# Performance work log

Hardware: AMD Instinct MI355X
Metric: run time of the kernel (lower is better)

The kernel has to match this reference:

```python
import jax, jax.numpy as jnp
import numpy as np

T, B, DIM = 64, 16, 512
H, Dh, ETA = 8, 64, 4
FD = ETA * Dh  # feature_dim = 256
EPS = 1e-6


def setup_inputs() -> dict:
    key = jax.random.key(0)
    ks = jax.random.split(key, 12)

    def w(k, o, i):
        return jax.random.normal(k, (o, i), jnp.float32) * (1.0 / np.sqrt(i).astype(np.float32))

    return {
        "inputs": jax.random.normal(ks[0], (T, B, DIM), jnp.float32),
        "terminations": jax.random.randint(ks[1], (T, B), 0, 2).astype(jnp.int32),
        "kv_state_prev": jnp.zeros((B, H, FD, Dh), jnp.float32),
        "norm_state_prev": jnp.zeros((B, H, FD), jnp.float32),
        "Wq": w(ks[2], H * Dh, DIM),
        "Wk": w(ks[3], H * Dh, DIM),
        "Wv": w(ks[4], H * Dh, DIM),
        "Wb": w(ks[5], H * Dh, DIM),
        "Wg": w(ks[6], H * Dh, DIM),
        "Wp1": w(ks[7], H * ETA, DIM),
        "Wp2": w(ks[8], H * ETA, DIM),
        "Wp3": w(ks[9], H * ETA, DIM),
        "Wo": w(ks[10], DIM, H * Dh),
        "bo": jnp.zeros((DIM,), jnp.float32),
    }


def reference(inputs, terminations, kv_state_prev, norm_state_prev,
              Wq, Wk, Wv, Wb, Wg, Wp1, Wp2, Wp3, Wo, bo):
    def proj(W, e):
        return (inputs @ W.T).reshape(T, B, H, e)

    q = proj(Wq, Dh)
    k = proj(Wk, Dh)
    v = proj(Wv, Dh)
    beta = jax.nn.sigmoid(proj(Wb, Dh))
    gamma = jax.nn.sigmoid(proj(Wg, Dh))
    p1 = proj(Wp1, ETA)
    p2 = proj(Wp2, ETA)
    p3 = proj(Wp3, ETA)

    # feature map: outer product of relu(p) [eta] and x [head_dim] -> [eta*head_dim]
    def fmap(x, p):
        return jnp.einsum('tbhe,tbhd->tbhed', jax.nn.relu(p), x).reshape(T, B, H, FD)

    phi_q = fmap(q, p2)
    psi_k = fmap(k, p1)
    # gamma map: outer product of sigmoid(p3) and sigmoid-gated gamma, values in (0,1)
    gamma_feat = jnp.einsum('tbhe,tbhd->tbhed', jax.nn.sigmoid(p3), gamma).reshape(T, B, H, FD)

    gated_v = v * beta                       # [T,B,H,Dh]
    gated_k = psi_k * gamma_feat             # [T,B,H,FD]

    term_mask = (1.0 - terminations.astype(jnp.float32))[:, :, None, None]  # [T,B,1,1]
    discount = (1.0 - gamma_feat) * term_mask  # [T,B,H,FD]

    kv_upd = jnp.einsum('tbhd,tbhD->tbhDd', gated_v, gated_k)  # [T,B,H,FD,Dh]

    def step(carry, x):
        kv, nm = carry
        d, u_kv, u_nm = x
        kv = d[..., None] * kv + u_kv
        nm = d * nm + u_nm
        return (kv, nm), (kv, nm)

    _, (kv_all, nm_all) = jax.lax.scan(step, (kv_state_prev, norm_state_prev),
                                       (discount, kv_upd, gated_k))

    attn_num = jnp.einsum('tbhDd,tbhD->tbhd', kv_all, phi_q)
    attn_den = jnp.einsum('tbhD,tbhD->tbh', phi_q, nm_all)
    attn_out = (attn_num / (attn_den[..., None] + EPS)).reshape(T, B, H * Dh)
    output = attn_out @ Wo.T + bo
    return (output, kv_all[-1], nm_all[-1])
```

## Files before the change

kernel.cpp:

```cpp
#include <hip/hip_runtime.h>


#define T_N   64
#define B_N   16
#define DIM_N 512
#define H_N   8
#define DH_N  64

#define OUT_ELEMS   524288
#define KV_ELEMS    2097152
#define PROJ_ELEMS  2719744

typedef _Float16 f16;
typedef f16   f16x8 __attribute__((ext_vector_type(8)));
typedef float f32x4 __attribute__((ext_vector_type(4)));

__device__ __forceinline__ float sigmoidf_(float x) {
    return 1.0f / (1.0f + __expf(-x));
}

template <int CTRL, int RM>
__device__ __forceinline__ float dpp_add_(float x) {
    int mv = __builtin_amdgcn_update_dpp(__float_as_int(x), __float_as_int(x),
                                         CTRL, RM, 0xF, false);
    return x + __int_as_float(mv);
}
__device__ __forceinline__ float half_reduce_dpp(float x) {
    x = dpp_add_<0xB1, 0xF>(x);
    x = dpp_add_<0x4E, 0xF>(x);
    x = dpp_add_<0x141, 0xF>(x);
    x = dpp_add_<0x140, 0xF>(x);
    x = dpp_add_<0x142, 0xA>(x);
    return x;
}

__device__ __forceinline__ void gemm64_core(const float* __restrict__ A,
                                            const float* __restrict__ W,
                                            const float* __restrict__ bias,
                                            float* __restrict__ C, int N,
                                            int mb, int nb, int kBase, int kLen) {
    const int nbase = nb * 64;
    if (nbase >= N) return;

    __shared__ float As[2][16][68];
    __shared__ float Bs[2][16][68];

    const int tid = threadIdx.x;
    const int mbase = mb * 64;
    const int tx = tid & 15;
    const int ty = tid >> 4;
    const int sr = tid >> 2;
    const int sk = (tid & 3) << 2;
    const bool wok = (nbase + sr) < N;

    const float* Ap = A + (size_t)(mbase + sr) * 512 + kBase + sk;
    const float* Wp = W + (size_t)(nbase + sr) * 512 + kBase + sk;

    float4 av = *(const float4*)Ap;
    float4 wv = wok ? *(const float4*)Wp : make_float4(0.f, 0.f, 0.f, 0.f);
    As[0][sk + 0][sr] = av.x; As[0][sk + 1][sr] = av.y;
    As[0][sk + 2][sr] = av.z; As[0][sk + 3][sr] = av.w;
    Bs[0][sk + 0][sr] = wv.x; Bs[0][sk + 1][sr] = wv.y;
    Bs[0][sk + 2][sr] = wv.z; Bs[0][sk + 3][sr] = wv.w;

    float acc[4][4];
    #pragma unroll
    for (int i = 0; i < 4; ++i)
        #pragma unroll
        for (int j = 0; j < 4; ++j) acc[i][j] = 0.f;

    for (int k0 = 0; k0 < kLen; k0 += 16) {
        const int buf = (k0 >> 4) & 1;
        __syncthreads();
        const bool more = (k0 + 16) < kLen;
        if (more) {
            av = *(const float4*)(Ap + k0 + 16);
            wv = wok ? *(const float4*)(Wp + k0 + 16) : make_float4(0.f, 0.f, 0.f, 0.f);
        }
        #pragma unroll
        for (int k = 0; k < 16; ++k) {
            float4 a  = *(const float4*)&As[buf][k][ty << 2];
            float4 bq = *(const float4*)&Bs[buf][k][tx << 2];
            float ar[4] = {a.x, a.y, a.z, a.w};
            float br[4] = {bq.x, bq.y, bq.z, bq.w};
            #pragma unroll
            for (int i = 0; i < 4; ++i)
                #pragma unroll
                for (int j = 0; j < 4; ++j)
                    acc[i][j] = fmaf(ar[i], br[j], acc[i][j]);
        }
        if (more) {
            const int nbuf = buf ^ 1;
            As[nbuf][sk + 0][sr] = av.x; As[nbuf][sk + 1][sr] = av.y;
            As[nbuf][sk + 2][sr] = av.z; As[nbuf][sk + 3][sr] = av.w;
            Bs[nbuf][sk + 0][sr] = wv.x; Bs[nbuf][sk + 1][sr] = wv.y;
            Bs[nbuf][sk + 2][sr] = wv.z; Bs[nbuf][sk + 3][sr] = wv.w;
        }
    }

    #pragma unroll
    for (int i = 0; i < 4; ++i) {
        const int m = mbase + (ty << 2) + i;
        #pragma unroll
        for (int j = 0; j < 4; ++j) {
            const int n = nbase + (tx << 2) + j;
            if (n < N) {
                float v = acc[i][j];
                if (bias) v += bias[n];
                C[(size_t)m * N + n] = v;
            }
        }
    }
}

struct ProjW {
    const float* W[8];
    float*       D[8];
};

__device__ __forceinline__ void cvt_split_store(f16* __restrict__ dh,
                                                f16* __restrict__ dl,
                                                float4 v0, float4 v1) {
    float x[8] = {v0.x, v0.y, v0.z, v0.w, v1.x, v1.y, v1.z, v1.w};
    f16x8 h, lo;
    #pragma unroll
    for (int e = 0; e < 8; ++e) {
        f16 hh = (f16)x[e];
        h[e]  = hh;
        lo[e] = (f16)(x[e] - (float)hh);
    }
    *(f16x8*)dh = h;
    *(f16x8*)dl = lo;
}

__global__ __launch_bounds__(256) void proj_mfma_kernel(const float* __restrict__ X,
                                                        ProjW a) {
    const int id = blockIdx.x;
    const int z = id & 7;
    const int rem = id >> 3;
    const int mb = rem & 15;
    const int nb = rem >> 4;
    const int N = (z < 5) ? 512 : 32;
    const int nbase = nb * 64;
    if (nbase >= N) return;

    const float* __restrict__ W = a.W[z];
    float* __restrict__ C = a.D[z];
    const int mbase = mb * 64;

    __shared__ f16 AsH[2][64][40];
    __shared__ f16 AsL[2][64][40];
    __shared__ f16 BsH[2][64][40];
    __shared__ f16 BsL[2][64][40];

    const int tid = threadIdx.x;
    const int sr = tid >> 2;
    const int kq = (tid & 3) << 3;
    const bool wok = (nbase + sr) < N;
    const float* Ap = X + (size_t)(mbase + sr) * 512 + kq;
    const float* Wp = W + (size_t)(nbase + sr) * 512 + kq;

    const int l  = tid & 63;
    const int w  = tid >> 6;
    const int wr = (w >> 1) << 5;
    const int wc = (w & 1) << 5;
    const int lr = l & 15;
    const int lk = (l >> 4) << 3;

    f32x4 acc[2][2] = {};

    float4 xa0 = *(const float4*)(Ap);
    float4 xa1 = *(const float4*)(Ap + 4);
    float4 wb0 = wok ? *(const float4*)(Wp)     : make_float4(0.f, 0.f, 0.f, 0.f);
    float4 wb1 = wok ? *(const float4*)(Wp + 4) : make_float4(0.f, 0.f, 0.f, 0.f);
    cvt_split_store(&AsH[0][sr][kq], &AsL[0][sr][kq], xa0, xa1);
    cvt_split_store(&BsH[0][sr][kq], &BsL[0][sr][kq], wb0, wb1);

    for (int k0 = 0; k0 < 512; k0 += 32) {
        const int buf = (k0 >> 5) & 1;
        __syncthreads();
        const bool more = (k0 + 32) < 512;
        if (more) {
            xa0 = *(const float4*)(Ap + k0 + 32);
            xa1 = *(const float4*)(Ap + k0 + 36);
            wb0 = wok ? *(const float4*)(Wp + k0 + 32) : make_float4(0.f, 0.f, 0.f, 0.f);
            wb1 = wok ? *(const float4*)(Wp + k0 + 36) : make_float4(0.f, 0.f, 0.f, 0.f);
        }

        f16x8 aH[2], aL[2], bH[2], bL[2];
        #pragma unroll
        for (int i = 0; i < 2; ++i) {
            const int row = wr + i * 16 + lr;
            aH[i] = *(const f16x8*)&AsH[buf][row][lk];
            aL[i] = *(const f16x8*)&AsL[buf][row][lk];
        }
        #pragma unroll
        for (int j = 0; j < 2; ++j) {
            const int col = wc + j * 16 + lr;
            bH[j] = *(const f16x8*)&BsH[buf][col][lk];
            bL[j] = *(const f16x8*)&BsL[buf][col][lk];
        }

        #pragma unroll
        for (int i = 0; i < 2; ++i)
            #pragma unroll
            for (int j = 0; j < 2; ++j) {
                acc[i][j] = __builtin_amdgcn_mfma_f32_16x16x32_f16(aH[i], bH[j], acc[i][j], 0, 0, 0);
                acc[i][j] = __builtin_amdgcn_mfma_f32_16x16x32_f16(aH[i], bL[j], acc[i][j], 0, 0, 0);
                acc[i][j] = __builtin_amdgcn_mfma_f32_16x16x32_f16(aL[i], bH[j], acc[i][j], 0, 0, 0);
            }

        if (more) {
            const int nbuf = buf ^ 1;
            cvt_split_store(&AsH[nbuf][sr][kq], &AsL[nbuf][sr][kq], xa0, xa1);
            cvt_split_store(&BsH[nbuf][sr][kq], &BsL[nbuf][sr][kq], wb0, wb1);
        }
    }

    #pragma unroll
    for (int j = 0; j < 2; ++j) {
        const int n = nbase + wc + j * 16 + lr;
        if (n < N) {
            #pragma unroll
            for (int i = 0; i < 2; ++i) {
                #pragma unroll
                for (int q = 0; q < 4; ++q) {
                    const int m = mbase + wr + i * 16 + ((l >> 4) << 2) + q;
                    C[(size_t)m * N + n] = acc[i][j][q];
                }
            }
        }
    }
}

__global__ __launch_bounds__(256) void out_gemm_kernel(const float* __restrict__ A,
                                                       const float* __restrict__ W,
                                                       const float* __restrict__ bias,
                                                       float* __restrict__ C) {
    gemm64_core(A, W, bias, C, 512, blockIdx.x, blockIdx.y, 0, 512);
}

struct OutP { float* P[4]; };
__global__ __launch_bounds__(256) void out_partial_kernel(const float* __restrict__ A,
                                                          const float* __restrict__ W,
                                                          OutP p) {
    const int id = blockIdx.x;
    const int m = id & 15;
    const int n = (id >> 4) & 7;
    const int kq = id >> 7;
    gemm64_core(A, W, nullptr, p.P[kq], 512, m, n, kq * 128, 128);
}

__global__ __launch_bounds__(256) void out_reduce_kernel(
    const float* __restrict__ p0, const float* __restrict__ p1,
    const float* __restrict__ p2, const float* __restrict__ p3,
    const float* __restrict__ bias, float* __restrict__ out) {
    const int i = blockIdx.x * 256 + threadIdx.x;
    float4 a = ((const float4*)p0)[i];
    float4 b = ((const float4*)p1)[i];
    float4 c = ((const float4*)p2)[i];
    float4 d = ((const float4*)p3)[i];
    float4 bv = ((const float4*)bias)[i & 127];
    float4 r;
    r.x = a.x + b.x + c.x + d.x + bv.x;
    r.y = a.y + b.y + c.y + d.y + bv.y;
    r.z = a.z + b.z + c.z + d.z + bv.z;
    r.w = a.w + b.w + c.w + d.w + bv.w;
    ((float4*)out)[i] = r;
}

__global__ __launch_bounds__(256) void gate_kernel(
    const float* __restrict__ qb,  const float* __restrict__ kb,
    const float* __restrict__ vb,  const float* __restrict__ bb,
    const float* __restrict__ gb,  const float* __restrict__ p1b,
    const float* __restrict__ p2b, const float* __restrict__ p3b,
    const int* __restrict__ term,
    float* __restrict__ disc_g, float* __restrict__ gk_g,
    float* __restrict__ phiq_g, float* __restrict__ gv_g) {
    const int h = blockIdx.x;
    const int row = blockIdx.y;
    const int D = threadIdx.x;
    const int e = D >> 6, di = D & 63;
    const size_t base = (size_t)row * 512 + h * 64;
    const size_t pb = (size_t)row * 32 + h * 4;

    float q = qb[base + di], k = kb[base + di], g = gb[base + di];
    float p1 = p1b[pb + e], p2 = p2b[pb + e], p3 = p3b[pb + e];
    float mask = 1.0f - (float)term[row];
    float gf = sigmoidf_(p3) * sigmoidf_(g);

    const size_t o = ((size_t)row * 8 + h) * 256 + D;
    disc_g[o] = (1.0f - gf) * mask;
    gk_g[o]   = fmaxf(p1, 0.f) * k * gf;
    phiq_g[o] = fmaxf(p2, 0.f) * q;
    if (D < 64)
        gv_g[((size_t)row * 8 + h) * 64 + D] = vb[base + D] * sigmoidf_(bb[base + D]);
}

__global__ __launch_bounds__(256) void scan8_kernel(
    const float* __restrict__ disc_g, const float* __restrict__ gk_g,
    const float* __restrict__ phiq_g, const float* __restrict__ gv_g,
    float* __restrict__ vb ,
    const float* __restrict__ kv0, const float* __restrict__ nm0,
    float* __restrict__ dout) {
    const int blk = blockIdx.x;
    const int bh = blk & 127;
    const int s  = blk >> 7;
    const int b  = bh >> 3;
    const int h  = bh & 7;
    const int tid = threadIdx.x;
    const int w = tid >> 6;
    const int l = tid & 63;
    const int half = l >> 5;
    const int li = l & 31;
    const int d0 = s * 16 + w * 4 + half * 2;
    const int D0 = li << 3;

    float kv[8][2];
    float nm[8];
    {
        const float* kp = kv0 + ((size_t)bh * 256 + D0) * 64 + d0;
        #pragma unroll
        for (int j = 0; j < 8; ++j) {
            float2 r = *(const float2*)(kp + (size_t)j * 64);
            kv[j][0] = r.x; kv[j][1] = r.y;
        }
        float4 na  = *(const float4*)(nm0 + (size_t)bh * 256 + D0);
        float4 nb_ = *(const float4*)(nm0 + (size_t)bh * 256 + D0 + 4);
        nm[0] = na.x; nm[1] = na.y; nm[2] = na.z; nm[3] = na.w;
        nm[4] = nb_.x; nm[5] = nb_.y; nm[6] = nb_.z; nm[7] = nb_.w;
    }

    float4 cd0, cd1, cg0, cg1, cp0, cp1; float2 cgv;
    {
        const size_t go = ((size_t)b * 8 + h) * 256 + D0;
        cd0 = *(const float4*)(disc_g + go);  cd1 = *(const float4*)(disc_g + go + 4);
        cg0 = *(const float4*)(gk_g + go);    cg1 = *(const float4*)(gk_g + go + 4);
        cp0 = *(const float4*)(phiq_g + go);  cp1 = *(const float4*)(phiq_g + go + 4);
        cgv = *(const float2*)(gv_g + ((size_t)b * 8 + h) * 64 + d0);
    }

    for (int t = 0; t < T_N; ++t) {
        const int row = t * B_N + b;
        const size_t base = (size_t)row * 512 + h * 64;

        float4 nd0 = {}, nd1 = {}, ng0 = {}, ng1 = {}, np0 = {}, np1 = {};
        float2 ngv = {};
        if (t + 1 < T_N) {
            const size_t go2 = ((size_t)(row + B_N) * 8 + h) * 256 + D0;
            nd0 = *(const float4*)(disc_g + go2); nd1 = *(const float4*)(disc_g + go2 + 4);
            ng0 = *(const float4*)(gk_g + go2);   ng1 = *(const float4*)(gk_g + go2 + 4);
            np0 = *(const float4*)(phiq_g + go2); np1 = *(const float4*)(phiq_g + go2 + 4);
            ngv = *(const float2*)(gv_g + ((size_t)(row + B_N) * 8 + h) * 64 + d0);
        }

        const float dj[8]  = {cd0.x, cd0.y, cd0.z, cd0.w, cd1.x, cd1.y, cd1.z, cd1.w};
        const float gkj[8] = {cg0.x, cg0.y, cg0.z, cg0.w, cg1.x, cg1.y, cg1.z, cg1.w};
        const float phj[8] = {cp0.x, cp0.y, cp0.z, cp0.w, cp1.x, cp1.y, cp1.z, cp1.w};

        float den = 0.f, n0 = 0.f, n1 = 0.f;
        #pragma unroll
        for (int j = 0; j < 8; ++j) {
            nm[j] = dj[j] * nm[j] + gkj[j];
            den = fmaf(phj[j], nm[j], den);
            kv[j][0] = dj[j] * kv[j][0] + gkj[j] * cgv.x; n0 = fmaf(phj[j], kv[j][0], n0);
            kv[j][1] = dj[j] * kv[j][1] + gkj[j] * cgv.y; n1 = fmaf(phj[j], kv[j][1], n1);
        }

        n0  = half_reduce_dpp(n0);
        n1  = half_reduce_dpp(n1);
        den = half_reduce_dpp(den);

        if (li == 16) {
            vb[base + d0]     = n0 / (den + 1e-6f);
            vb[base + d0 + 1] = n1 / (den + 1e-6f);
        }

        cd0 = nd0; cd1 = nd1; cg0 = ng0; cg1 = ng1; cp0 = np0; cp1 = np1; cgv = ngv;
    }

    {
        float* kp = dout + OUT_ELEMS + ((size_t)bh * 256 + D0) * 64 + d0;
        #pragma unroll
        for (int j = 0; j < 8; ++j)
            *(float2*)(kp + (size_t)j * 64) = make_float2(kv[j][0], kv[j][1]);
        if (s == 0 && w == 0 && half == 0) {
            float* np = dout + OUT_ELEMS + KV_ELEMS + (size_t)bh * 256 + D0;
            *(float4*)np       = make_float4(nm[0], nm[1], nm[2], nm[3]);
            *(float4*)(np + 4) = make_float4(nm[4], nm[5], nm[6], nm[7]);
        }
    }
}

extern "C" void kernel_launch(void* const* d_in, const int* in_sizes, int n_in,
                              void* d_out, int out_size, void* d_ws, size_t ws_size,
                              hipStream_t stream) {
    (void)in_sizes; (void)n_in; (void)out_size;

    const float* X    = (const float*)d_in[0];
    const int*   term = (const int*)  d_in[1];
    const float* kv0  = (const float*)d_in[2];
    const float* nm0  = (const float*)d_in[3];
    const float* Wo   = (const float*)d_in[12];
    const float* bo   = (const float*)d_in[13];

    float* out = (float*)d_out;

    float* qb  = (float*)d_ws;
    float* kb  = qb  + 524288;
    float* vb  = kb  + 524288;
    float* bb  = vb  + 524288;
    float* gb  = bb  + 524288;
    float* p1b = gb  + 524288;
    float* p2b = p1b + 32768;
    float* p3b = p2b + 32768;
    float* disc_g = p3b + 32768;
    float* gk_g   = disc_g + 2097152;
    float* phiq_g = gk_g   + 2097152;
    float* gv_g   = phiq_g + 2097152;
    const size_t need_bytes = (size_t)(PROJ_ELEMS + 6815744) * 4;
    const bool big = ws_size >= need_bytes;

    ProjW pa;
    pa.W[0] = (const float*)d_in[4];  pa.W[1] = (const float*)d_in[5];
    pa.W[2] = (const float*)d_in[6];  pa.W[3] = (const float*)d_in[7];
    pa.W[4] = (const float*)d_in[8];  pa.W[5] = (const float*)d_in[9];
    pa.W[6] = (const float*)d_in[10]; pa.W[7] = (const float*)d_in[11];
    pa.D[0] = qb;  pa.D[1] = kb;  pa.D[2] = vb;  pa.D[3] = bb;
    pa.D[4] = gb;  pa.D[5] = p1b; pa.D[6] = p2b; pa.D[7] = p3b;
    proj_mfma_kernel<<<1024, 256, 0, stream>>>(X, pa);

    gate_kernel<<<dim3(8, 1024), 256, 0, stream>>>(qb, kb, vb, bb, gb,
                                                   p1b, p2b, p3b, term,
                                                   disc_g, gk_g, phiq_g, gv_g);
    scan8_kernel<<<512, 256, 0, stream>>>(disc_g, gk_g, phiq_g, gv_g,
                                          vb, kv0, nm0, out);
    if (big) {
        OutP op; op.P[0] = qb; op.P[1] = kb; op.P[2] = bb; op.P[3] = gb;
        out_partial_kernel<<<512, 256, 0, stream>>>(vb, Wo, op);
        out_reduce_kernel<<<512, 256, 0, stream>>>(qb, kb, bb, gb, bo, out);
    } else {
        out_gemm_kernel<<<dim3(16, 8), 256, 0, stream>>>(vb, Wo, bo, out);
    }
}
```

Baseline: 175.8 us.

## Fuse gate computation into scan kernel via double-buffered shared memory

```diff
diff --git a/kernel.cpp b/kernel.cpp
--- a/kernel.cpp
+++ b/kernel.cpp
@@ -269,38 +269,15 @@
     ((float4*)out)[i] = r;
 }
 
-__global__ __launch_bounds__(256) void gate_kernel(
-    const float* __restrict__ qb,  const float* __restrict__ kb,
-    const float* __restrict__ vb,  const float* __restrict__ bb,
-    const float* __restrict__ gb,  const float* __restrict__ p1b,
+#define WIDX(D) ((D) + (((D) >> 3) << 2))
+
+__global__ __launch_bounds__(256) void scan11_kernel(
+    const float* __restrict__ qb, const float* __restrict__ kb,
+    const float* __restrict__ vbi, const float* __restrict__ bb,
+    const float* __restrict__ gb, const float* __restrict__ p1b,
     const float* __restrict__ p2b, const float* __restrict__ p3b,
     const int* __restrict__ term,
-    float* __restrict__ disc_g, float* __restrict__ gk_g,
-    float* __restrict__ phiq_g, float* __restrict__ gv_g) {
-    const int h = blockIdx.x;
-    const int row = blockIdx.y;
-    const int D = threadIdx.x;
-    const int e = D >> 6, di = D & 63;
-    const size_t base = (size_t)row * 512 + h * 64;
-    const size_t pb = (size_t)row * 32 + h * 4;
-
-    float q = qb[base + di], k = kb[base + di], g = gb[base + di];
-    float p1 = p1b[pb + e], p2 = p2b[pb + e], p3 = p3b[pb + e];
-    float mask = 1.0f - (float)term[row];
-    float gf = sigmoidf_(p3) * sigmoidf_(g);
-
-    const size_t o = ((size_t)row * 8 + h) * 256 + D;
-    disc_g[o] = (1.0f - gf) * mask;
-    gk_g[o]   = fmaxf(p1, 0.f) * k * gf;
-    phiq_g[o] = fmaxf(p2, 0.f) * q;
-    if (D < 64)
-        gv_g[((size_t)row * 8 + h) * 64 + D] = vb[base + D] * sigmoidf_(bb[base + D]);
-}
-
-__global__ __launch_bounds__(256) void scan8_kernel(
-    const float* __restrict__ disc_g, const float* __restrict__ gk_g,
-    const float* __restrict__ phiq_g, const float* __restrict__ gv_g,
-    float* __restrict__ vb ,
+    float* __restrict__ attn ,
     const float* __restrict__ kv0, const float* __restrict__ nm0,
     float* __restrict__ dout) {
     const int blk = blockIdx.x;
@@ -316,6 +293,14 @@
     const int d0 = s * 16 + w * 4 + half * 2;
     const int D0 = li << 3;
 
+    __shared__ float Sd[2][384];
+    __shared__ float Sg[2][384];
+    __shared__ float Sp[2][384];
+    __shared__ float Sv[2][64];
+
+    const int gdi = tid & 63;
+    const int ge  = tid >> 6;
+
     float kv[8][2];
     float nm[8];
     {
@@ -331,28 +316,46 @@
         nm[4] = nb_.x; nm[5] = nb_.y; nm[6] = nb_.z; nm[7] = nb_.w;
     }
 
-    float4 cd0, cd1, cg0, cg1, cp0, cp1; float2 cgv;
     {
-        const size_t go = ((size_t)b * 8 + h) * 256 + D0;
-        cd0 = *(const float4*)(disc_g + go);  cd1 = *(const float4*)(disc_g + go + 4);
-        cg0 = *(const float4*)(gk_g + go);    cg1 = *(const float4*)(gk_g + go + 4);
-        cp0 = *(const float4*)(phiq_g + go);  cp1 = *(const float4*)(phiq_g + go + 4);
-        cgv = *(const float2*)(gv_g + ((size_t)b * 8 + h) * 64 + d0);
-    }
+        const size_t base = (size_t)b * 512 + h * 64;
+        const size_t pb = (size_t)b * 32 + h * 4 + ge;
+        float k0 = kb[base + gdi], g0 = gb[base + gdi], q0 = qb[base + gdi];
+        float p1 = p1b[pb], p2 = p2b[pb], p3 = p3b[pb];
+        float mask = 1.0f - (float)term[b];
+        float gf = sigmoidf_(p3) * sigmoidf_(g0);
+        const int wi = WIDX(tid);
+        Sd[0][wi] = (1.0f - gf) * mask;
+        Sg[0][wi] = fmaxf(p1, 0.f) * k0 * gf;
+        Sp[0][wi] = fmaxf(p2, 0.f) * q0;
+        if (tid < 64) Sv[0][tid] = vbi[base + tid] * sigmoidf_(bb[base + tid]);
+    }
+    __syncthreads();
+
+    const int rbase = WIDX(D0);
 
     for (int t = 0; t < T_N; ++t) {
+        const int cur = t & 1, nxt = cur ^ 1;
         const int row = t * B_N + b;
-        const size_t base = (size_t)row * 512 + h * 64;
-
-        float4 nd0 = {}, nd1 = {}, ng0 = {}, ng1 = {}, np0 = {}, np1 = {};
-        float2 ngv = {};
-        if (t + 1 < T_N) {
-            const size_t go2 = ((size_t)(row + B_N) * 8 + h) * 256 + D0;
-            nd0 = *(const float4*)(disc_g + go2); nd1 = *(const float4*)(disc_g + go2 + 4);
-            ng0 = *(const float4*)(gk_g + go2);   ng1 = *(const float4*)(gk_g + go2 + 4);
-            np0 = *(const float4*)(phiq_g + go2); np1 = *(const float4*)(phiq_g + go2 + 4);
-            ngv = *(const float2*)(gv_g + ((size_t)(row + B_N) * 8 + h) * 64 + d0);
-        }
+        const bool more = (t + 1) < T_N;
+
+        float rk = 0.f, rg = 0.f, rq = 0.f, rp1 = 0.f, rp2 = 0.f, rp3 = 0.f;
+        float rmask = 0.f, rv = 0.f, rb_ = 0.f;
+        if (more) {
+            const size_t nbase = (size_t)(row + B_N) * 512 + h * 64;
+            const size_t npb = (size_t)(row + B_N) * 32 + h * 4 + ge;
+            rk = kb[nbase + gdi]; rg = gb[nbase + gdi]; rq = qb[nbase + gdi];
+            rp1 = p1b[npb]; rp2 = p2b[npb]; rp3 = p3b[npb];
+            rmask = 1.0f - (float)term[row + B_N];
+            if (tid < 64) { rv = vbi[nbase + tid]; rb_ = bb[nbase + tid]; }
+        }
+
+        float4 cd0 = *(const float4*)&Sd[cur][rbase];
+        float4 cd1 = *(const float4*)&Sd[cur][rbase + 4];
+        float4 cg0 = *(const float4*)&Sg[cur][rbase];
+        float4 cg1 = *(const float4*)&Sg[cur][rbase + 4];
+        float4 cp0 = *(const float4*)&Sp[cur][rbase];
+        float4 cp1 = *(const float4*)&Sp[cur][rbase + 4];
+        float2 cgv = *(const float2*)&Sv[cur][d0];
 
         const float dj[8]  = {cd0.x, cd0.y, cd0.z, cd0.w, cd1.x, cd1.y, cd1.z, cd1.w};
         const float gkj[8] = {cg0.x, cg0.y, cg0.z, cg0.w, cg1.x, cg1.y, cg1.z, cg1.w};
@@ -372,11 +375,20 @@
         den = half_reduce_dpp(den);
 
         if (li == 16) {
-            vb[base + d0]     = n0 / (den + 1e-6f);
-            vb[base + d0 + 1] = n1 / (den + 1e-6f);
-        }
-
-        cd0 = nd0; cd1 = nd1; cg0 = ng0; cg1 = ng1; cp0 = np0; cp1 = np1; cgv = ngv;
+            const size_t obase = (size_t)row * 512 + h * 64;
+            attn[obase + d0]     = n0 / (den + 1e-6f);
+            attn[obase + d0 + 1] = n1 / (den + 1e-6f);
+        }
+
+        if (more) {
+            float gf = sigmoidf_(rp3) * sigmoidf_(rg);
+            const int wi = WIDX(tid);
+            Sd[nxt][wi] = (1.0f - gf) * rmask;
+            Sg[nxt][wi] = fmaxf(rp1, 0.f) * rk * gf;
+            Sp[nxt][wi] = fmaxf(rp2, 0.f) * rq;
+            if (tid < 64) Sv[nxt][tid] = rv * sigmoidf_(rb_);
+        }
+        __syncthreads();
     }
 
     {
@@ -414,10 +426,7 @@
     float* p1b = gb  + 524288;
     float* p2b = p1b + 32768;
     float* p3b = p2b + 32768;
-    float* disc_g = p3b + 32768;
-    float* gk_g   = disc_g + 2097152;
-    float* phiq_g = gk_g   + 2097152;
-    float* gv_g   = phiq_g + 2097152;
+    float* attn = p3b + 32768;
     const size_t need_bytes = (size_t)(PROJ_ELEMS + 6815744) * 4;
     const bool big = ws_size >= need_bytes;
 
@@ -430,16 +439,14 @@
     pa.D[4] = gb;  pa.D[5] = p1b; pa.D[6] = p2b; pa.D[7] = p3b;
     proj_mfma_kernel<<<1024, 256, 0, stream>>>(X, pa);
 
-    gate_kernel<<<dim3(8, 1024), 256, 0, stream>>>(qb, kb, vb, bb, gb,
-                                                   p1b, p2b, p3b, term,
-                                                   disc_g, gk_g, phiq_g, gv_g);
-    scan8_kernel<<<512, 256, 0, stream>>>(disc_g, gk_g, phiq_g, gv_g,
-                                          vb, kv0, nm0, out);
+    scan11_kernel<<<512, 256, 0, stream>>>(qb, kb, vb, bb, gb,
+                                           p1b, p2b, p3b, term,
+                                           attn, kv0, nm0, out);
     if (big) {
         OutP op; op.P[0] = qb; op.P[1] = kb; op.P[2] = bb; op.P[3] = gb;
-        out_partial_kernel<<<512, 256, 0, stream>>>(vb, Wo, op);
+        out_partial_kernel<<<512, 256, 0, stream>>>(attn, Wo, op);
         out_reduce_kernel<<<512, 256, 0, stream>>>(qb, kb, bb, gb, bo, out);
     } else {
-        out_gemm_kernel<<<dim3(16, 8), 256, 0, stream>>>(vb, Wo, bo, out);
-    }
-}
+        out_gemm_kernel<<<dim3(16, 8), 256, 0, stream>>>(attn, Wo, bo, out);
+    }
+}
```

Result: slower. 188.2 us (+7.1%).
